# Kernel optimization log

Measured on AMD Instinct MI355X. Metric: run time of the kernel, lower is better.

## Reference

```python
import jax, jax.numpy as jnp
import numpy as np

N_HEAD = 16
ROPE_BASE = 10000.0


def _rope_cos_sin(T, D, dtype):
    # inv_freq over even dims, freqs concatenated twice (rotate_half convention)
    inv_freq = 1.0 / (ROPE_BASE ** (jnp.arange(0, D, 2, dtype=jnp.float32) / D))
    t = jnp.arange(T, dtype=jnp.float32)
    freqs = jnp.outer(t, inv_freq)          # [T, D/2]
    emb = jnp.concatenate([freqs, freqs], axis=-1)  # [T, D]
    return jnp.cos(emb).astype(dtype), jnp.sin(emb).astype(dtype)


def _rotate_half(x):
    x1, x2 = jnp.split(x, 2, axis=-1)
    return jnp.concatenate([-x2, x1], axis=-1)


def setup_inputs() -> dict:
    key = jax.random.key(0)
    ks = jax.random.split(key, 5)
    B, T, C = 2, 2048, 1024
    s = 1.0 / np.sqrt(C)
    return {
        "x": jax.random.normal(ks[0], (B, T, C), jnp.float32),
        "W_attn": jax.random.normal(ks[1], (C, 3 * C), jnp.float32) * s,
        "b_attn": jax.random.normal(ks[2], (3 * C,), jnp.float32) * 0.02,
        "W_proj": jax.random.normal(ks[3], (C, C), jnp.float32) * s,
        "b_proj": jax.random.normal(ks[4], (C,), jnp.float32) * 0.02,
    }


def reference(x, W_attn, b_attn, W_proj, b_proj):
    B, T, C = x.shape
    H = N_HEAD
    D = C // H

    # fused QKV projection
    qkv = x @ W_attn + b_attn                      # [B, T, 3C]
    q, k, v = jnp.split(qkv, 3, axis=-1)
    q = q.reshape(B, T, H, D).transpose(0, 2, 1, 3)  # [B, H, T, D]
    k = k.reshape(B, T, H, D).transpose(0, 2, 1, 3)
    v = v.reshape(B, T, H, D).transpose(0, 2, 1, 3)

    # RoPE (no past_kv: applied to full q and k)
    cos, sin = _rope_cos_sin(T, D, x.dtype)        # [T, D]
    cos = cos[None, None]                          # [1, 1, T, D]
    sin = sin[None, None]
    q = q * cos + _rotate_half(q) * sin
    k = k * cos + _rotate_half(k) * sin

    # causal SDPA (dropout_p = 0 in reference)
    scale = 1.0 / np.sqrt(D)
    scores = jnp.einsum("bhqd,bhkd->bhqk", q, k) * scale
    causal = jnp.tril(jnp.ones((T, T), dtype=bool))
    scores = jnp.where(causal, scores, jnp.finfo(scores.dtype).min)
    attn = jax.nn.softmax(scores, axis=-1)
    y = jnp.einsum("bhqk,bhkd->bhqd", attn, v)     # [B, H, T, D]

    y = y.transpose(0, 2, 1, 3).reshape(B, T, C)
    y = y @ W_proj + b_proj
    return y
```

## Files before the change

### kernel.cpp

```cpp
#include <hip/hip_runtime.h>
#include <cstdint>
#include <cstddef>

#define SEQ_T 2048
#define NHEAD 16

typedef __attribute__((ext_vector_type(8))) short short8;
typedef __attribute__((ext_vector_type(4))) float f32x4;
typedef __attribute__((ext_vector_type(16))) float f32x16;

__device__ __forceinline__ unsigned short f2bf(float f) {
  union { float f; unsigned int u; } v; v.f = f;
  return (unsigned short)((v.u + 0x7FFFu + ((v.u >> 16) & 1u)) >> 16);
}

__device__ __forceinline__ unsigned cvtpk(float lo, float hi) {
  unsigned r;
  asm("v_cvt_pk_bf16_f32 %0, %1, %2" : "=v"(r) : "v"(lo), "v"(hi));
  return r;
}

#if __has_builtin(__builtin_amdgcn_permlane32_swap)
__device__ __forceinline__ void plswap(unsigned& a, unsigned& b) {
  auto r = __builtin_amdgcn_permlane32_swap(a, b, false, false);
  a = r[0];
  b = r[1];
}
#else
__device__ __forceinline__ void plswap(unsigned& a, unsigned& b) {
  asm volatile("s_nop 1\n\tv_permlane32_swap_b32 %0, %1\n\ts_nop 1"
               : "+v"(a), "+v"(b));
}
#endif

__device__ __forceinline__ float xhalf_max(float x) {
  unsigned a = __builtin_bit_cast(unsigned, x), b = a;
  plswap(a, b);
  return fmaxf(__builtin_bit_cast(float, a), __builtin_bit_cast(float, b));
}
__device__ __forceinline__ float xhalf_add(float x) {
  unsigned a = __builtin_bit_cast(unsigned, x), b = a;
  plswap(a, b);
  return __builtin_bit_cast(float, a) + __builtin_bit_cast(float, b);
}

__device__ __forceinline__ float vmax16(const f32x16 v) {
  float a0 = fmaxf(v[0], v[8]),  a1 = fmaxf(v[1], v[9]);
  float a2 = fmaxf(v[2], v[10]), a3 = fmaxf(v[3], v[11]);
  float a4 = fmaxf(v[4], v[12]), a5 = fmaxf(v[5], v[13]);
  float a6 = fmaxf(v[6], v[14]), a7 = fmaxf(v[7], v[15]);
  float b0 = fmaxf(a0, a4), b1 = fmaxf(a1, a5);
  float b2 = fmaxf(a2, a6), b3 = fmaxf(a3, a7);
  return fmaxf(fmaxf(b0, b1), fmaxf(b2, b3));
}

__device__ __forceinline__ void gl_lds16(const void* g, void* l) {
  __builtin_amdgcn_global_load_lds(
      (__attribute__((address_space(1))) void*)(void*)g,
      (__attribute__((address_space(3))) void*)l, 16, 0, 0);
}

__global__ void k_prep(const float* __restrict__ x,
                       const float* __restrict__ Wa,
                       const float* __restrict__ Wp,
                       unsigned short* __restrict__ xb,
                       unsigned short* __restrict__ wat,
                       unsigned short* __restrict__ wpt,
                       float2* __restrict__ tab) {
  const int b = blockIdx.x, tid = threadIdx.x;
  if (b < 4096) {
    int i = b * 256 + tid;
    float4 v = ((const float4*)x)[i];
    unsigned long long pk = (unsigned long long)f2bf(v.x)
                          | ((unsigned long long)f2bf(v.y) << 16)
                          | ((unsigned long long)f2bf(v.z) << 32)
                          | ((unsigned long long)f2bf(v.w) << 48);
    ((unsigned long long*)xb)[i] = pk;
  } else if (b < 5632) {
    int idx = (b - 4096) * 256 + tid;
    int n = idx % 3072, k0 = (idx / 3072) * 8;
    short8 v;
#pragma unroll
    for (int j = 0; j < 8; ++j)
      v[j] = (short)f2bf(Wa[(size_t)(k0 + j) * 3072 + n]);
    *(short8*)&wat[(size_t)n * 1024 + k0] = v;
  } else if (b < 6144) {
    int idx = (b - 5632) * 256 + tid;
    int n = idx & 1023, k0 = (idx >> 10) * 8;
    short8 v;
#pragma unroll
    for (int j = 0; j < 8; ++j)
      v[j] = (short)f2bf(Wp[(size_t)(k0 + j) * 1024 + n]);
    *(short8*)&wpt[(size_t)n * 1024 + k0] = v;
  } else {
    int idx = (b - 6144) * 256 + tid;
    int t = idx >> 5, i = idx & 31;
    float inv = powf(10000.0f, -(float)(2 * i) / 64.0f);
    float f = (float)t * inv;
    tab[idx] = make_float2(cosf(f), sinf(f));
  }
}

__global__ void k_gemm_qkv(const unsigned short* __restrict__ A,
                           const unsigned short* __restrict__ Bt,
                           const float* __restrict__ bias,
                           const float2* __restrict__ cs,
                           unsigned short* __restrict__ qo,
                           unsigned short* __restrict__ ko,
                           unsigned short* __restrict__ vo) {
  __shared__ unsigned short lA[128 * 32];
  __shared__ unsigned short lB[128 * 32];
  const int K = 1024;
  const int bn = blockIdx.x, bm = blockIdx.y;
  const int tid = threadIdx.x, w = tid >> 6, l = tid & 63;
  const int lr = l & 15, lh = l >> 4;
  const int wm = w >> 1, wn = w & 1;

  f32x4 acc[4][4];
#pragma unroll
  for (int m = 0; m < 4; ++m)
#pragma unroll
    for (int n = 0; n < 4; ++n)
#pragma unroll
      for (int i = 0; i < 4; ++i) acc[m][n][i] = 0.f;

  const unsigned short* ga0 = A + (size_t)(bm * 128 + w * 16 + (l >> 2)) * K + (l & 3) * 8;
  const unsigned short* gb0 = Bt + (size_t)(bn * 128 + w * 16 + (l >> 2)) * K + (l & 3) * 8;
  unsigned short* la0 = &lA[w * 512];
  unsigned short* la1 = &lA[(w + 4) * 512];
  unsigned short* lb0 = &lB[w * 512];
  unsigned short* lb1 = &lB[(w + 4) * 512];

  for (int kt = 0; kt < K; kt += 32) {
    gl_lds16(ga0 + kt, la0);
    gl_lds16(ga0 + (size_t)64 * K + kt, la1);
    gl_lds16(gb0 + kt, lb0);
    gl_lds16(gb0 + (size_t)64 * K + kt, lb1);
    __syncthreads();
    short8 af[4], bf[4];
#pragma unroll
    for (int m = 0; m < 4; ++m) af[m] = *(const short8*)&lA[(wm * 64 + m * 16 + lr) * 32 + lh * 8];
#pragma unroll
    for (int n = 0; n < 4; ++n) bf[n] = *(const short8*)&lB[(wn * 64 + n * 16 + lr) * 32 + lh * 8];
#pragma unroll
    for (int m = 0; m < 4; ++m)
#pragma unroll
      for (int n = 0; n < 4; ++n)
        acc[m][n] = __builtin_amdgcn_mfma_f32_16x16x32_bf16(af[m], bf[n], acc[m][n], 0, 0, 0);
    __syncthreads();
  }

  const int col0 = bn * 128 + wn * 64;
  const int row0 = bm * 128 + wm * 64;
  const int sec = col0 >> 10;
  const int hh = (col0 >> 6) & 15;
  float bl[4];
#pragma unroll
  for (int n = 0; n < 4; ++n) bl[n] = bias[col0 + n * 16 + lr];

  if (sec == 2) {
    const int b = row0 >> 11;
    unsigned short* vtp = vo + (size_t)(b * 16 + hh) * 64 * 2048;
#pragma unroll
    for (int n = 0; n < 4; ++n) {
      int d = n * 16 + lr;
#pragma unroll
      for (int m = 0; m < 4; ++m) {
        int t = (row0 + m * 16 + lh * 4) & 2047;
        unsigned long long pk = (unsigned long long)f2bf(acc[m][n][0] + bl[n])
                              | ((unsigned long long)f2bf(acc[m][n][1] + bl[n]) << 16)
                              | ((unsigned long long)f2bf(acc[m][n][2] + bl[n]) << 32)
                              | ((unsigned long long)f2bf(acc[m][n][3] + bl[n]) << 48);
        *(unsigned long long*)&vtp[(size_t)d * 2048 + t] = pk;
      }
    }
  } else {
    unsigned short* dst = (sec == 0) ? qo : ko;
#pragma unroll
    for (int m = 0; m < 4; ++m)
#pragma unroll
      for (int i = 0; i < 4; ++i) {
        int row = row0 + m * 16 + lh * 4 + i;
        int t = row & 2047, b = row >> 11;
        size_t ob = ((size_t)(b * 16 + hh) * 2048 + t) * 64;
#pragma unroll
        for (int n = 0; n < 4; ++n) {
          float v = acc[m][n][i] + bl[n];
          float pv = acc[m][n ^ 2][i] + bl[n ^ 2];
          int d = n * 16 + lr;
          float2 c = cs[t * 32 + (d & 31)];
          float rot = (d < 32) ? -pv : pv;
          dst[ob + d] = f2bf(v * c.x + rot * c.y);
        }
      }
  }
}

__global__ __launch_bounds__(512, 4) void k_attn(const unsigned short* __restrict__ Q,
                       const unsigned short* __restrict__ Kg,
                       const unsigned short* __restrict__ VT,
                       unsigned short* __restrict__ O) {
  __shared__ unsigned short kl[3][64 * 64];
  __shared__ unsigned short vl[3][64 * 64];
  const int id = blockIdx.x;
  const int xcd = id & 7, u = id >> 3;
  const int g = u >> 4;
  const int bh = xcd * 4 + g;
  const int s = (u + g * 4) & 15;
  const int qt = (s & 1) ? 15 - (s >> 1) : (s >> 1);
  const int tid = threadIdx.x, w = tid >> 6, l = tid & 63;
  const int wq = w & 3, wk = w >> 2;
  const int lq = l & 31, hi = l >> 5;
  const size_t base = (size_t)bh * SEQ_T * 64;
  const float CE = 0.18033688f;
  const float DTHR = 44.3614f;

  const int qrow = qt * 128 + wq * 32 + lq;
  short8 qf[4];
#pragma unroll
  for (int c = 0; c < 4; ++c)
    qf[c] = *(const short8*)&Q[base + (size_t)qrow * 64 + c * 16 + hi * 8];

  const int r0 = tid >> 3, c8 = tid & 7;
  const unsigned short* ks0 = Kg + base + (size_t)r0 * 64 + ((c8 ^ (r0 & 7)) * 8);
  const unsigned short* vs0 = VT + base + (size_t)r0 * 2048 + ((c8 ^ (r0 & 7)) * 8);

#define STAGE(KT, B) do { \
    gl_lds16(ks0 + (size_t)(KT) * 4096, &kl[B][w * 512]); \
    gl_lds16(vs0 + (size_t)(KT) * 64,   &vl[B][w * 512]); \
  } while (0)

#define QKSTEP(KB, ST) do { \
    const unsigned short* kb_ = &kl[KB][0]; \
    _Pragma("unroll") \
    for (int c_ = 0; c_ < 4; ++c_) { \
      const short8 kf_ = *(const short8*)&kb_[(wk * 32 + lq) * 64 + (((2 * c_ + hi) ^ (lq & 7)) * 8)]; \
      ST = __builtin_amdgcn_mfma_f32_32x32x16_bf16(kf_, qf[c_], ST, 0, 0, 0); \
    } \
  } while (0)

  float mi = -1.0e30f, li = 0.f;
  f32x16 oc0, oc1, stC, stN;
#pragma unroll
  for (int r = 0; r < 16; ++r) { oc0[r] = 0.f; oc1[r] = 0.f; stC[r] = 0.f; }

  const int nkt = 2 * qt + 2;
  STAGE(0, 0);
  STAGE(1, 1);
  __syncthreads();
  QKSTEP(0, stC);

  for (int kt = 0; kt < nkt; ++kt) {
    if (kt + 2 < nkt) STAGE(kt + 2, (kt + 2) % 3);

    if (kt + 1 < nkt) {
#pragma unroll
      for (int r = 0; r < 16; ++r) stN[r] = 0.f;
      QKSTEP((kt + 1) % 3, stN);
    }

    if (kt >= nkt - 2) {
#pragma unroll
      for (int r = 0; r < 16; ++r) {
        int kvg = kt * 64 + wk * 32 + (r & 3) + 8 * (r >> 2) + 4 * hi;
        if (kvg > qrow) stC[r] = -3.0e38f;
      }
    }

    float tm = xhalf_max(vmax16(stC));
    if (!__all(tm <= mi + DTHR)) {
      float mn = fmaxf(mi, tm);
      float scq = exp2f((mi - mn) * CE);
      mi = mn;
      li *= scq;
#pragma unroll
      for (int r = 0; r < 16; ++r) {
        float sc_r = __shfl(scq, (r & 3) + 8 * (r >> 2) + 4 * hi, 64);
        oc0[r] *= sc_r;
        oc1[r] *= sc_r;
      }
    }
    const float nb = mi * CE;
    float rs = 0.f;
#pragma unroll
    for (int r = 0; r < 16; ++r) {
      float p = exp2f(fmaf(stC[r], CE, -nb));
      stC[r] = p;
      rs += p;
    }
    li += xhalf_add(rs);

    short8 pa[2];
#pragma unroll
    for (int kc = 0; kc < 2; ++kc) {
      const int o = kc * 8;
      unsigned w0 = cvtpk(stC[o + 0], stC[o + 1]);
      unsigned w1 = cvtpk(stC[o + 2], stC[o + 3]);
      unsigned w2 = cvtpk(stC[o + 4], stC[o + 5]);
      unsigned w3 = cvtpk(stC[o + 6], stC[o + 7]);
      plswap(w0, w2);
      plswap(w1, w3);
      uint4 F;
      F.x = w0; F.y = w1; F.z = w2; F.w = w3;
      pa[kc] = __builtin_bit_cast(short8, F);
    }

    {
      const unsigned short* vb_ = &vl[kt % 3][0];
      short8 vbf[2][2];
#pragma unroll
      for (int dt = 0; dt < 2; ++dt)
#pragma unroll
        for (int kc = 0; kc < 2; ++kc)
          vbf[dt][kc] = *(const short8*)&vb_[(dt * 32 + lq) * 64 +
                          (((wk * 4 + kc * 2 + hi) ^ (lq & 7)) * 8)];
      __builtin_amdgcn_s_setprio(1);
#pragma unroll
      for (int kc = 0; kc < 2; ++kc) {
        oc0 = __builtin_amdgcn_mfma_f32_32x32x16_bf16(pa[kc], vbf[0][kc], oc0, 0, 0, 0);
        oc1 = __builtin_amdgcn_mfma_f32_32x32x16_bf16(pa[kc], vbf[1][kc], oc1, 0, 0, 0);
      }
      __builtin_amdgcn_s_setprio(0);
    }

    stC = stN;
    if (kt + 1 < nkt) __syncthreads();
  }

  __syncthreads();
  float* obuf = (float*)&kl[0][0];
  float* mlb  = (float*)&vl[2][0];
  if (wk == 1) {
#pragma unroll
    for (int r = 0; r < 16; ++r) {
      const int q = (r & 3) + 8 * (r >> 2) + 4 * hi;
      obuf[wq * 2048 + q * 64 + lq]      = oc0[r];
      obuf[wq * 2048 + q * 64 + 32 + lq] = oc1[r];
    }
    if (hi == 0) {
      mlb[wq * 64 + lq * 2 + 0] = mi;
      mlb[wq * 64 + lq * 2 + 1] = li;
    }
  }
  __syncthreads();
  if (wk == 0) {
    const int hh = bh & 15, bb = bh >> 4;
#pragma unroll
    for (int r = 0; r < 16; ++r) {
      const int q = (r & 3) + 8 * (r >> 2) + 4 * hi;
      float m0 = __shfl(mi, q, 64), l0 = __shfl(li, q, 64);
      float m1 = mlb[wq * 64 + q * 2 + 0], l1 = mlb[wq * 64 + q * 2 + 1];
      float mm = fmaxf(m0, m1);
      float f0 = exp2f((m0 - mm) * CE), f1 = exp2f((m1 - mm) * CE);
      float inv = 1.0f / (f0 * l0 + f1 * l1);
      float o0 = (f0 * oc0[r] + f1 * obuf[wq * 2048 + q * 64 + lq]) * inv;
      float o1 = (f0 * oc1[r] + f1 * obuf[wq * 2048 + q * 64 + 32 + lq]) * inv;
      int qg = qt * 128 + wq * 32 + q;
      size_t ob = (size_t)(bb * 2048 + qg) * 1024 + hh * 64;
      O[ob + lq]      = f2bf(o0);
      O[ob + 32 + lq] = f2bf(o1);
    }
  }
#undef STAGE
#undef QKSTEP
}

__global__ void k_gemm_proj(const unsigned short* __restrict__ A,
                            const unsigned short* __restrict__ Bt,
                            const float* __restrict__ bias,
                            float* __restrict__ out) {
  __shared__ unsigned short lA[128 * 32];
  __shared__ unsigned short lB[128 * 32];
  const int K = 1024;
  const int bn = blockIdx.x, bm = blockIdx.y;
  const int tid = threadIdx.x, w = tid >> 6, l = tid & 63;
  const int lr = l & 15, lh = l >> 4;
  const int wm = w >> 1, wn = w & 1;

  f32x4 acc[4][4];
#pragma unroll
  for (int m = 0; m < 4; ++m)
#pragma unroll
    for (int n = 0; n < 4; ++n)
#pragma unroll
      for (int i = 0; i < 4; ++i) acc[m][n][i] = 0.f;

  const unsigned short* ga0 = A + (size_t)(bm * 128 + w * 16 + (l >> 2)) * K + (l & 3) * 8;
  const unsigned short* gb0 = Bt + (size_t)(bn * 128 + w * 16 + (l >> 2)) * K + (l & 3) * 8;
  unsigned short* la0 = &lA[w * 512];
  unsigned short* la1 = &lA[(w + 4) * 512];
  unsigned short* lb0 = &lB[w * 512];
  unsigned short* lb1 = &lB[(w + 4) * 512];

  for (int kt = 0; kt < K; kt += 32) {
    gl_lds16(ga0 + kt, la0);
    gl_lds16(ga0 + (size_t)64 * K + kt, la1);
    gl_lds16(gb0 + kt, lb0);
    gl_lds16(gb0 + (size_t)64 * K + kt, lb1);
    __syncthreads();
    short8 af[4], bf[4];
#pragma unroll
    for (int m = 0; m < 4; ++m) af[m] = *(const short8*)&lA[(wm * 64 + m * 16 + lr) * 32 + lh * 8];
#pragma unroll
    for (int n = 0; n < 4; ++n) bf[n] = *(const short8*)&lB[(wn * 64 + n * 16 + lr) * 32 + lh * 8];
#pragma unroll
    for (int m = 0; m < 4; ++m)
#pragma unroll
      for (int n = 0; n < 4; ++n)
        acc[m][n] = __builtin_amdgcn_mfma_f32_16x16x32_bf16(af[m], bf[n], acc[m][n], 0, 0, 0);
    __syncthreads();
  }

  const int col0 = bn * 128 + wn * 64;
  const int row0 = bm * 128 + wm * 64;
  float bl[4];
#pragma unroll
  for (int n = 0; n < 4; ++n) bl[n] = bias[col0 + n * 16 + lr];
#pragma unroll
  for (int m = 0; m < 4; ++m)
#pragma unroll
    for (int i = 0; i < 4; ++i) {
      int row = row0 + m * 16 + lh * 4 + i;
#pragma unroll
      for (int n = 0; n < 4; ++n)
        out[(size_t)row * 1024 + col0 + n * 16 + lr] = acc[m][n][i] + bl[n];
    }
}

extern "C" void kernel_launch(void* const* d_in, const int* in_sizes, int n_in,
                              void* d_out, int out_size, void* d_ws, size_t ws_size,
                              hipStream_t stream) {
  const float* x     = (const float*)d_in[0];
  const float* Wattn = (const float*)d_in[1];
  const float* battn = (const float*)d_in[2];
  const float* Wproj = (const float*)d_in[3];
  const float* bproj = (const float*)d_in[4];
  float* out = (float*)d_out;

  char* ws = (char*)d_ws;
  unsigned short* xb  = (unsigned short*)(ws);
  unsigned short* wat = (unsigned short*)(ws + (8ull  << 20));
  unsigned short* wpt = (unsigned short*)(ws + (14ull << 20));
  unsigned short* qa  = (unsigned short*)(ws + (16ull << 20));
  unsigned short* ka  = (unsigned short*)(ws + (24ull << 20));
  unsigned short* va  = (unsigned short*)(ws + (32ull << 20));
  unsigned short* ob  = (unsigned short*)(ws + (40ull << 20));
  float2* cs          = (float2*)(ws + (48ull << 20));

  k_prep<<<6400, 256, 0, stream>>>(x, Wattn, Wproj, xb, wat, wpt, cs);
  k_gemm_qkv<<<dim3(24, 32), 256, 0, stream>>>(xb, wat, battn, cs, qa, ka, va);
  k_attn<<<512, 512, 0, stream>>>(qa, ka, va, ob);
  k_gemm_proj<<<dim3(8, 32), 256, 0, stream>>>(ob, wpt, bproj, out);
}
```

Before: 140.2 us.

## Split attention KV range across two blocks and merge partials in combine kernel

The attention kernel now launches twice as many blocks. Each handles half of a query tile's causal KV range and writes partial bf16 outputs plus per-row max and denominator. A new combine kernel merges the two halves with log-sum-exp weights, reusing dead workspace buffers (xb, wat) for the second partial and the stats. The pipeline also drops from three LDS stages with QK lookahead to double buffering. The aim is more parallelism and a shorter critical path per block, at the cost of an extra kernel launch, extra memory traffic and an extra bf16 rounding of the partials.

```diff
diff --git a/kernel.cpp b/kernel.cpp
--- a/kernel.cpp
+++ b/kernel.cpp
@@ -12,6 +12,10 @@
 __device__ __forceinline__ unsigned short f2bf(float f) {
   union { float f; unsigned int u; } v; v.f = f;
   return (unsigned short)((v.u + 0x7FFFu + ((v.u >> 16) & 1u)) >> 16);
+}
+__device__ __forceinline__ float bf2f(unsigned short u) {
+  union { unsigned int u; float f; } v; v.u = ((unsigned int)u) << 16;
+  return v.f;
 }
 
 __device__ __forceinline__ unsigned cvtpk(float lo, float hi) {
@@ -199,15 +203,17 @@
 __global__ __launch_bounds__(512, 4) void k_attn(const unsigned short* __restrict__ Q,
                        const unsigned short* __restrict__ Kg,
                        const unsigned short* __restrict__ VT,
-                       unsigned short* __restrict__ O) {
-  __shared__ unsigned short kl[3][64 * 64];
-  __shared__ unsigned short vl[3][64 * 64];
+                       unsigned short* __restrict__ P0,
+                       unsigned short* __restrict__ P1,
+                       float2* __restrict__ ML) {
+  __shared__ unsigned short smem[16896];
   const int id = blockIdx.x;
   const int xcd = id & 7, u = id >> 3;
-  const int g = u >> 4;
+  const int a = u & 31, sweep = u >> 5;
+  const int g = a & 3, j = a >> 2;
   const int bh = xcd * 4 + g;
-  const int s = (u + g * 4) & 15;
-  const int qt = (s & 1) ? 15 - (s >> 1) : (s >> 1);
+  const int qt = (sweep & 1) ? (15 - j) : j;
+  const int sp = sweep >> 1;
   const int tid = threadIdx.x, w = tid >> 6, l = tid & 63;
   const int wq = w & 3, wk = w >> 2;
   const int lq = l & 31, hi = l >> 5;
@@ -226,48 +232,48 @@
   const unsigned short* vs0 = VT + base + (size_t)r0 * 2048 + ((c8 ^ (r0 & 7)) * 8);
 
 #define STAGE(KT, B) do { \
-    gl_lds16(ks0 + (size_t)(KT) * 4096, &kl[B][w * 512]); \
-    gl_lds16(vs0 + (size_t)(KT) * 64,   &vl[B][w * 512]); \
+    gl_lds16(ks0 + (size_t)(KT) * 4096, &smem[(B) * 4096 + w * 512]); \
+    gl_lds16(vs0 + (size_t)(KT) * 64,   &smem[8192 + (B) * 4096 + w * 512]); \
   } while (0)
 
-#define QKSTEP(KB, ST) do { \
-    const unsigned short* kb_ = &kl[KB][0]; \
-    _Pragma("unroll") \
-    for (int c_ = 0; c_ < 4; ++c_) { \
-      const short8 kf_ = *(const short8*)&kb_[(wk * 32 + lq) * 64 + (((2 * c_ + hi) ^ (lq & 7)) * 8)]; \
-      ST = __builtin_amdgcn_mfma_f32_32x32x16_bf16(kf_, qf[c_], ST, 0, 0, 0); \
-    } \
-  } while (0)
-
   float mi = -1.0e30f, li = 0.f;
-  f32x16 oc0, oc1, stC, stN;
-#pragma unroll
-  for (int r = 0; r < 16; ++r) { oc0[r] = 0.f; oc1[r] = 0.f; stC[r] = 0.f; }
-
-  const int nkt = 2 * qt + 2;
-  STAGE(0, 0);
-  STAGE(1, 1);
+  f32x16 oc0, oc1;
+#pragma unroll
+  for (int r = 0; r < 16; ++r) { oc0[r] = 0.f; oc1[r] = 0.f; }
+
+  const int nit = qt + 1;
+  const int kt0 = sp * nit;
+  const int mfrom = 2 * qt;
+  STAGE(kt0, 0);
   __syncthreads();
-  QKSTEP(0, stC);
-
-  for (int kt = 0; kt < nkt; ++kt) {
-    if (kt + 2 < nkt) STAGE(kt + 2, (kt + 2) % 3);
-
-    if (kt + 1 < nkt) {
-#pragma unroll
-      for (int r = 0; r < 16; ++r) stN[r] = 0.f;
-      QKSTEP((kt + 1) % 3, stN);
-    }
-
-    if (kt >= nkt - 2) {
+
+  for (int it = 0; it < nit; ++it) {
+    const int cur = it & 1;
+    const int kt = kt0 + it;
+    if (it + 1 < nit) STAGE(kt + 1, cur ^ 1);
+    const unsigned short* kb = &smem[cur * 4096];
+    const unsigned short* vb = &smem[8192 + cur * 4096];
+
+    f32x16 st;
+#pragma unroll
+    for (int r = 0; r < 16; ++r) st[r] = 0.f;
+    __builtin_amdgcn_s_setprio(1);
+#pragma unroll
+    for (int c = 0; c < 4; ++c) {
+      const short8 kf = *(const short8*)&kb[(wk * 32 + lq) * 64 + (((2 * c + hi) ^ (lq & 7)) * 8)];
+      st = __builtin_amdgcn_mfma_f32_32x32x16_bf16(kf, qf[c], st, 0, 0, 0);
+    }
+    __builtin_amdgcn_s_setprio(0);
+
+    if (kt >= mfrom) {
 #pragma unroll
       for (int r = 0; r < 16; ++r) {
         int kvg = kt * 64 + wk * 32 + (r & 3) + 8 * (r >> 2) + 4 * hi;
-        if (kvg > qrow) stC[r] = -3.0e38f;
+        if (kvg > qrow) st[r] = -3.0e38f;
       }
     }
 
-    float tm = xhalf_max(vmax16(stC));
+    float tm = xhalf_max(vmax16(st));
     if (!__all(tm <= mi + DTHR)) {
       float mn = fmaxf(mi, tm);
       float scq = exp2f((mi - mn) * CE);
@@ -284,8 +290,8 @@
     float rs = 0.f;
 #pragma unroll
     for (int r = 0; r < 16; ++r) {
-      float p = exp2f(fmaf(stC[r], CE, -nb));
-      stC[r] = p;
+      float p = exp2f(fmaf(st[r], CE, -nb));
+      st[r] = p;
       rs += p;
     }
     li += xhalf_add(rs);
@@ -294,10 +300,10 @@
 #pragma unroll
     for (int kc = 0; kc < 2; ++kc) {
       const int o = kc * 8;
-      unsigned w0 = cvtpk(stC[o + 0], stC[o + 1]);
-      unsigned w1 = cvtpk(stC[o + 2], stC[o + 3]);
-      unsigned w2 = cvtpk(stC[o + 4], stC[o + 5]);
-      unsigned w3 = cvtpk(stC[o + 6], stC[o + 7]);
+      unsigned w0 = cvtpk(st[o + 0], st[o + 1]);
+      unsigned w1 = cvtpk(st[o + 2], st[o + 3]);
+      unsigned w2 = cvtpk(st[o + 4], st[o + 5]);
+      unsigned w3 = cvtpk(st[o + 6], st[o + 7]);
       plswap(w0, w2);
       plswap(w1, w3);
       uint4 F;
@@ -306,13 +312,12 @@
     }
 
     {
-      const unsigned short* vb_ = &vl[kt % 3][0];
       short8 vbf[2][2];
 #pragma unroll
       for (int dt = 0; dt < 2; ++dt)
 #pragma unroll
         for (int kc = 0; kc < 2; ++kc)
-          vbf[dt][kc] = *(const short8*)&vb_[(dt * 32 + lq) * 64 +
+          vbf[dt][kc] = *(const short8*)&vb[(dt * 32 + lq) * 64 +
                           (((wk * 4 + kc * 2 + hi) ^ (lq & 7)) * 8)];
       __builtin_amdgcn_s_setprio(1);
 #pragma unroll
@@ -323,13 +328,12 @@
       __builtin_amdgcn_s_setprio(0);
     }
 
-    stC = stN;
-    if (kt + 1 < nkt) __syncthreads();
+    if (it + 1 < nit) __syncthreads();
   }
 
   __syncthreads();
-  float* obuf = (float*)&kl[0][0];
-  float* mlb  = (float*)&vl[2][0];
+  float* obuf = (float*)smem;
+  float* mlb  = (float*)&smem[16384];
   if (wk == 1) {
 #pragma unroll
     for (int r = 0; r < 16; ++r) {
@@ -344,6 +348,7 @@
   }
   __syncthreads();
   if (wk == 0) {
+    unsigned short* dst = sp ? P1 : P0;
     const int hh = bh & 15, bb = bh >> 4;
 #pragma unroll
     for (int r = 0; r < 16; ++r) {
@@ -352,17 +357,42 @@
       float m1 = mlb[wq * 64 + q * 2 + 0], l1 = mlb[wq * 64 + q * 2 + 1];
       float mm = fmaxf(m0, m1);
       float f0 = exp2f((m0 - mm) * CE), f1 = exp2f((m1 - mm) * CE);
-      float inv = 1.0f / (f0 * l0 + f1 * l1);
+      float dn = f0 * l0 + f1 * l1;
+      float inv = (dn > 0.f) ? (1.0f / dn) : 0.f;
       float o0 = (f0 * oc0[r] + f1 * obuf[wq * 2048 + q * 64 + lq]) * inv;
       float o1 = (f0 * oc1[r] + f1 * obuf[wq * 2048 + q * 64 + 32 + lq]) * inv;
       int qg = qt * 128 + wq * 32 + q;
       size_t ob = (size_t)(bb * 2048 + qg) * 1024 + hh * 64;
-      O[ob + lq]      = f2bf(o0);
-      O[ob + 32 + lq] = f2bf(o1);
+      dst[ob + lq]      = f2bf(o0);
+      dst[ob + 32 + lq] = f2bf(o1);
+      if (lq == 0) ML[(size_t)(sp * 32 + bh) * 2048 + qg] = make_float2(mm, dn);
     }
   }
 #undef STAGE
-#undef QKSTEP
+}
+
+__global__ void k_combine(const unsigned short* __restrict__ P1,
+                          const float2* __restrict__ ML,
+                          unsigned short* __restrict__ P0) {
+  const float CE = 0.18033688f;
+  int idx = blockIdx.x * 256 + threadIdx.x;
+  int flat = idx * 8;
+  int c = flat & 1023, t = (flat >> 10) & 2047, b = flat >> 21;
+  int bh = b * 16 + (c >> 6);
+  float2 a0 = ML[(size_t)bh * 2048 + t];
+  float2 a1 = ML[(size_t)(32 + bh) * 2048 + t];
+  float mm = fmaxf(a0.x, a1.x);
+  float w0 = exp2f((a0.x - mm) * CE) * a0.y;
+  float w1 = exp2f((a1.x - mm) * CE) * a1.y;
+  float inv = 1.0f / (w0 + w1);
+  w0 *= inv; w1 *= inv;
+  short8 o0 = *(const short8*)&P0[flat];
+  short8 o1 = *(const short8*)&P1[flat];
+  short8 o;
+#pragma unroll
+  for (int k = 0; k < 8; ++k)
+    o[k] = (short)f2bf(w0 * bf2f((unsigned short)o0[k]) + w1 * bf2f((unsigned short)o1[k]));
+  *(short8*)&P0[flat] = o;
 }
 
 __global__ void k_gemm_proj(const unsigned short* __restrict__ A,
@@ -446,9 +476,11 @@
   unsigned short* va  = (unsigned short*)(ws + (32ull << 20));
   unsigned short* ob  = (unsigned short*)(ws + (40ull << 20));
   float2* cs          = (float2*)(ws + (48ull << 20));
+  float2* ml          = (float2*)wat;
 
   k_prep<<<6400, 256, 0, stream>>>(x, Wattn, Wproj, xb, wat, wpt, cs);
   k_gemm_qkv<<<dim3(24, 32), 256, 0, stream>>>(xb, wat, battn, cs, qa, ka, va);
-  k_attn<<<512, 512, 0, stream>>>(qa, ka, va, ob);
+  k_attn<<<1024, 512, 0, stream>>>(qa, ka, va, ob, xb, ml);
+  k_combine<<<2048, 256, 0, stream>>>(xb, ml, ob);
   k_gemm_proj<<<dim3(8, 32), 256, 0, stream>>>(ob, wpt, bproj, out);
 }
```

Result: faster. 131.5 us (-6.2%).
